# Performance work log

Measured on AMD Instinct MI355X. Metric: run time of the kernel, lower is better.

Reference implementation:

```python
import jax, jax.numpy as jnp
import numpy as np

NPAD = 50      # npadding from init
N_ITER = 5     # fixed Newton iteration count (torch uses tol-based early stop)
LR = 0.5


def conv_subspace(raw, kernel, npadding):
    # raw: (ntrial, nneuron, nt_full); kernel: (ntau, nsubspace)
    ntrial, nneuron, nt = raw.shape
    # enforce causality: prepend a zero tap
    k = jnp.concatenate([jnp.zeros((1, kernel.shape[1]), kernel.dtype), kernel], axis=0)
    ntau = k.shape[0]
    nfft = nt + ntau - 1
    Rf = jnp.fft.rfft(raw, n=nfft, axis=2)[..., None]          # (m, n, F, 1)
    Kf = jnp.fft.rfft(k, n=nfft, axis=0)[None, None, :, :]     # (1, 1, F, s)
    G = jnp.fft.irfft(Rf * Kf, n=nfft, axis=2)                 # (m, n, nfft, s)
    G = jnp.where(jnp.abs(G) < 1e-5, 0.0, G)                   # thresholding as in torch
    G = G[:, :, npadding:nt, :]                                # keep causal part, drop padding
    return jnp.swapaxes(G, -1, -2)                             # (m, n, s, T)


def setup_inputs() -> dict:
    key = jax.random.key(0)
    k1, k2, k3 = jax.random.split(key, 3)
    ntrial, nneuron, nt_full = 16, 96, 350
    T, nsub, ntau, nlat = 300, 8, 20, 8
    # spike counts
    Y_raw = jax.random.randint(k1, (ntrial, nneuron, nt_full), 0, 4).astype(jnp.float32)
    kernel = 0.02 * jax.random.normal(k2, (ntau, nsub), jnp.float32)
    w_proj = 0.05 * jax.random.normal(k3, (nsub, nlat), jnp.float32)
    # smooth RBF latent prior covariance (PSD, as a GP kernel K must be)
    t = jnp.arange(T, dtype=jnp.float32)
    K = jnp.exp(-(t[:, None] - t[None, :]) ** 2 / (2.0 * 20.0 ** 2))
    bias = jnp.float32(0.5)
    return {"Y_raw": Y_raw, "kernel": kernel, "w_proj": w_proj, "K": K, "bias": bias}


def reference(Y_raw, kernel, w_proj, K, bias):
    # FFT causal conv -> subspace signals -> per-neuron latent loading weights
    G = conv_subspace(Y_raw, kernel, NPAD)                     # (m, n, s, T)
    weights = jnp.einsum('mnst,sl->mnlt', G, w_proj)           # (m, n, L, T)
    Y = Y_raw[:, :, NPAD:]                                     # (m, n, T)
    m, n, L, T = weights.shape
    I = jnp.eye(T, dtype=K.dtype)
    inv_K = jnp.linalg.inv(K + 1e-3 * I)                       # (T, T)
    mu = jnp.zeros((m, L, T), Y.dtype)
    hessian = jnp.broadcast_to(inv_K, (m, L, T, T))            # torch init: +inv_K repeated
    w2 = weights ** 2
    for _ in range(N_ITER):
        log_lambd = jnp.einsum('mnlt,mlt->mnt', weights, mu) + bias
        h_inv = jnp.linalg.inv(hessian)                        # batched (m*L) TxT inverse
        dh = jnp.diagonal(h_inv, axis1=-2, axis2=-1)           # (m, L, T)
        lambd = jnp.exp(log_lambd + 0.5 * jnp.einsum('mlt,mnlt->mnt', dh, w2))
        grad = jnp.einsum('mnlt,mnt->mlt', weights, Y - lambd) - jnp.einsum('mlt,ts->mls', mu, inv_K)
        d = jnp.einsum('mnlt,mnt->mlt', w2, lambd)             # (m, L, T)
        hessian = -inv_K - d[..., :, None] * I                 # -inv_K - diag(d)
        mu = mu - LR * jnp.linalg.solve(hessian, grad[..., None])[..., 0]
    return mu
```

## Files before the change

kernel.cpp:

```cpp
#include <hip/hip_runtime.h>
#include <math.h>

namespace {
constexpr int Mb   = 16;
constexpr int Nn   = 96;
constexpr int NTF  = 350;
constexpr int Tt   = 300;
constexpr int NSUB = 8;
constexpr int NTAU = 20;
constexpr int NL   = 8;
constexpr int ML   = Mb * NL;
constexpr int R_   = 32;
constexpr int CS   = 33;
constexpr int CL   = 34;
constexpr int LDW  = 33;
constexpr int TP   = 320;
constexpr int CROWS= 384;
constexpr int NSIT = 12;
constexpr float EPS = 0.001f;
}

__device__ __forceinline__ int PIV(int k) { return (600 * k + 300) >> 6; }

__device__ __forceinline__ float  sqrt_(float x)  { return sqrtf(x); }
__device__ __forceinline__ double sqrt_(double x) { return sqrt(x); }

__device__ __forceinline__ void lfence() {
  asm volatile("s_waitcnt lgkmcnt(0)" ::: "memory");
}

template <typename T>
__device__ void chol32_trtri32(T* A, T* W, T* rd, T* V, int tid) {
  if (tid < 32) {
    const int r = tid;
    for (int c = 0; c < 32; ++c) {
      T dotp = (T)0, dotv = (T)0;
      for (int k = 0; k < c; ++k) {
        const T bc = A[c * LDW + k];
        dotp += bc * bc;
        dotv += A[r * LDW + k] * bc;
      }
      const T pivot = A[c * LDW + c] - dotp;
      T s, is;
      if (pivot > (T)1e-12) { s = sqrt_(pivot); is = (T)1 / s; }
      else                  { s = (T)0;         is = (T)0; }
      if (r == c)      { A[c * LDW + c] = s; rd[c] = is; }
      else if (r > c)  A[r * LDW + c] = (A[r * LDW + c] - dotv) * is;
      lfence();
    }
  }
  __syncthreads();
  if (tid < 32) {
    const int c = tid;
    V[c * LDW + c] = rd[c];
    for (int r = c + 1; r < 32; ++r) {
      T acc = (T)0;
      for (int k = c; k < r; ++k) acc += A[r * LDW + k] * V[k * LDW + c];
      V[r * LDW + c] = -acc * rd[r];
    }
    for (int r = 0; r < 32; ++r)
      W[r * LDW + c] = (r < c) ? (T)0 : V[r * LDW + c];
  }
  __syncthreads();
}

__global__ __launch_bounds__(256) void k_weights(
    const float* __restrict__ Yraw, const float* __restrict__ kern,
    const float* __restrict__ wproj, float* __restrict__ WA,
    float* __restrict__ Yt) {
  __shared__ float sk[NTAU * NSUB];
  __shared__ float sp[NSUB * NL];
  const int tid = threadIdx.x;
  if (tid < NTAU * NSUB) sk[tid] = kern[tid];
  if (tid < NSUB * NL)   sp[tid] = wproj[tid];
  __syncthreads();
  const int g = blockIdx.x * 256 + tid;
  if (g >= Mb * Tt * Nn) return;
  const int n  = g % Nn;
  const int mt = g / Nn;
  const int t  = mt % Tt;
  const int m  = mt / Tt;
  const float* yr = Yraw + ((size_t)m * Nn + n) * NTF + 30 + t;
  float ya[NTAU + 1];
#pragma unroll
  for (int j = 0; j <= NTAU; ++j) ya[j] = yr[j];
  float gs[NSUB];
#pragma unroll
  for (int s = 0; s < NSUB; ++s) {
    float acc = 0.f;
#pragma unroll
    for (int j = 0; j < NTAU; ++j) acc += ya[j] * sk[(NTAU - 1 - j) * NSUB + s];
    gs[s] = (fabsf(acc) < 1e-5f) ? 0.f : acc;
  }
  float w[NL];
#pragma unroll
  for (int l = 0; l < NL; ++l) {
    float acc = 0.f;
#pragma unroll
    for (int s = 0; s < NSUB; ++s) acc += gs[s] * sp[s * NL + l];
    w[l] = acc;
  }
  float4* wa4 = reinterpret_cast<float4*>(WA + (size_t)g * NL);
  wa4[0] = make_float4(w[0], w[1], w[2], w[3]);
  wa4[1] = make_float4(w[4], w[5], w[6], w[7]);
  Yt[g] = ya[NTAU];
}

__global__ __launch_bounds__(256) void k_scholM(
    const float* __restrict__ K, double* __restrict__ WS64) {
  __shared__ double A[R_ * LDW];
  __shared__ double V[R_ * LDW];
  __shared__ double rd[R_];
  const int tid = threadIdx.x;
  for (int e = tid; e < R_ * R_; e += 256) {
    const int a = e >> 5, b = e & 31;
    A[a * LDW + b] = (double)K[(size_t)PIV(a) * Tt + PIV(b)];
  }
  __syncthreads();
  chol32_trtri32<double>(A, WS64, rd, V, tid);
}

__global__ __launch_bounds__(320) void k_cmake(
    const float* __restrict__ K, const double* __restrict__ WS64,
    float* __restrict__ Cg) {
  const int k = blockIdx.x;
  const int t = threadIdx.x;
  if (k == R_) {
    for (int r = t; r < CROWS; r += 320) Cg[(size_t)r * CS + R_] = 0.f;
    return;
  }
  __shared__ double wrow[R_];
  if (t < R_) wrow[t] = WS64[(size_t)k * LDW + t];
  __syncthreads();
  if (t < Tt) {
    double acc = 0.0;
    for (int j = 0; j <= k; ++j)
      acc += wrow[j] * (double)K[(size_t)PIV(j) * Tt + t];
    Cg[(size_t)t * CS + k] = (float)acc;
  }
  for (int r = Tt + t; r < CROWS; r += 320) Cg[(size_t)r * CS + k] = 0.f;
}

__global__ __launch_bounds__(256) void k_rmul(
    const float* __restrict__ Cg, double* __restrict__ R64) {
  const int e = blockIdx.x * 256 + threadIdx.x;
  if (e >= R_ * R_) return;
  const int i = e >> 5, j = e & 31;
  double acc = (i == j) ? 0.001 : 0.0;
  for (int r = 0; r < Tt; ++r)
    acc += (double)Cg[(size_t)r * CS + i] * (double)Cg[(size_t)r * CS + j];
  R64[e] = acc;
}

__global__ __launch_bounds__(256) void k_qchol(
    const double* __restrict__ R64, double* __restrict__ W64) {
  __shared__ double A[R_ * LDW];
  __shared__ double V[R_ * LDW];
  __shared__ double rd[R_];
  const int tid = threadIdx.x;
  for (int e = tid; e < R_ * R_; e += 256) {
    const int i = e >> 5, j = e & 31;
    A[i * LDW + j] = R64[e];
  }
  __syncthreads();
  chol32_trtri32<double>(A, W64, rd, V, tid);
}

__global__ __launch_bounds__(256) void k_qmul(
    const double* __restrict__ W64, double* __restrict__ Qg) {
  const int e = blockIdx.x * 256 + threadIdx.x;
  if (e >= R_ * R_) return;
  const int i = e >> 5, j = e & 31;
  const int k0 = (i > j) ? i : j;
  double acc = 0.0;
  for (int k = k0; k < R_; ++k) acc += W64[k * LDW + i] * W64[k * LDW + j];
  Qg[e] = acc;
}

__global__ __launch_bounds__(256) void k_init(
    float* __restrict__ mu, float* __restrict__ dh) {
  const int g = blockIdx.x * 256 + threadIdx.x;
  if (g >= Mb * Tt * NL) return;
  mu[g] = 0.f;
  dh[g] = 1.0f + EPS;
}

__global__ __launch_bounds__(256) void k_gd2(
    const float* __restrict__ WA, const float* __restrict__ Yt,
    const float* __restrict__ mug, const float* __restrict__ dhg,
    const float* __restrict__ biasp, float* __restrict__ g1,
    float* __restrict__ dvec) {
  const int wg = blockIdx.x;
  const int m = wg / 10, ch = wg - m * 10;
  const int t0 = ch * 30;
  const int tid = threadIdx.x;
  __shared__ float pg[30 * 8 * 8];
  __shared__ float pd[30 * 8 * 8];
  if (tid < 240) {
    const int tl = tid >> 3, nq = tid & 7;
    const int t = t0 + tl;
    const float b = biasp[0];
    const float4* mp = reinterpret_cast<const float4*>(mug + ((size_t)m * Tt + t) * NL);
    const float4* dp = reinterpret_cast<const float4*>(dhg + ((size_t)m * Tt + t) * NL);
    const float4 m0 = mp[0], m1 = mp[1], h0 = dp[0], h1 = dp[1];
    const float mv[8] = {m0.x, m0.y, m0.z, m0.w, m1.x, m1.y, m1.z, m1.w};
    const float hv[8] = {0.5f * h0.x, 0.5f * h0.y, 0.5f * h0.z, 0.5f * h0.w,
                         0.5f * h1.x, 0.5f * h1.y, 0.5f * h1.z, 0.5f * h1.w};
    float ga[8], dd[8];
#pragma unroll
    for (int l = 0; l < 8; ++l) { ga[l] = 0.f; dd[l] = 0.f; }
    const float* war = WA + ((size_t)m * Tt + t) * Nn * NL;
    const float* ytr = Yt + ((size_t)m * Tt + t) * Nn;
    for (int i = 0; i < 12; ++i) {
      const int n = nq + 8 * i;
      const float4* w4 = reinterpret_cast<const float4*>(war + n * NL);
      const float4 w0 = w4[0], w1 = w4[1];
      const float wv[8] = {w0.x, w0.y, w0.z, w0.w, w1.x, w1.y, w1.z, w1.w};
      float e = b;
#pragma unroll
      for (int l = 0; l < 8; ++l) e += wv[l] * (mv[l] + wv[l] * hv[l]);
      const float lamn = expf(e);
      const float dy = ytr[n] - lamn;
#pragma unroll
      for (int l = 0; l < 8; ++l) {
        ga[l] += wv[l] * dy;
        dd[l] += wv[l] * wv[l] * lamn;
      }
    }
#pragma unroll
    for (int l = 0; l < 8; ++l) {
      pg[(tl * 8 + l) * 8 + nq] = ga[l];
      pd[(tl * 8 + l) * 8 + nq] = dd[l];
    }
  }
  __syncthreads();
  if (tid < 240) {
    const int tl = tid >> 3, l = tid & 7;
    float sg_ = 0.f, sd_ = 0.f;
#pragma unroll
    for (int nq = 0; nq < 8; ++nq) {
      sg_ += pg[(tl * 8 + l) * 8 + nq];
      sd_ += pd[(tl * 8 + l) * 8 + nq];
    }
    const size_t idx = (size_t)(m * NL + l) * TP + (t0 + tl);
    g1[idx]   = sg_;
    dvec[idx] = sd_;
  }
}

__global__ __launch_bounds__(320) void k_sys2(
    const float* __restrict__ Cg, const double* __restrict__ Qg,
    const float* __restrict__ g1, const float* __restrict__ dvec,
    float* __restrict__ mug, float* __restrict__ dhg) {
  const int ml = blockIdx.x;
  const int mt = ml / NL, lat = ml % NL;
  const int tid = threadIdx.x;
  __shared__ float  Cf[Tt * CL];
  __shared__ float  M[R_ * LDW];
  __shared__ float  Xa[R_ * LDW];
  __shared__ float  Xb[R_ * LDW];
  __shared__ float  T[R_ * LDW];
  __shared__ float  muv[Tt], gv[Tt], sv[Tt], dl[Tt], sg[Tt];
  __shared__ double pv[R_], qv[R_];
  __shared__ double pB[R_ * 10];
  __shared__ float  pU[R_ * 10];
  __shared__ float  uv[R_], yv[R_];
  __shared__ float  red[R_ + 2];
  for (int e = tid; e < Tt * CS; e += 320) {
    const int r = e / CS, c = e - r * CS;
    Cf[r * CL + c] = Cg[e];
  }
  if (tid < Tt) {
    const float m_ = mug[((size_t)mt * Tt + tid) * NL + lat];
    const float g_ = g1[(size_t)ml * TP + tid];
    const float d_ = dvec[(size_t)ml * TP + tid];
    muv[tid] = m_; gv[tid] = g_;
    const float s = 1.f / (1.f + EPS * d_);
    sv[tid] = s;
    dl[tid] = d_ * s;
  }
  __syncthreads();
  {
    const int k = tid & 31, ch = tid >> 5;
    double acc = 0.0;
    const int ta = ch * 30;
    for (int t = ta; t < ta + 30; ++t)
      acc += (double)Cf[t * CL + k] * (double)muv[t];
    pB[k * 10 + ch] = acc;
  }
  __syncthreads();
  if (tid < R_) {
    double a = 0.0;
    for (int ch = 0; ch < 10; ++ch) a += pB[tid * 10 + ch];
    pv[tid] = a;
  }
  __syncthreads();
  if (tid < R_) {
    double acc = 0.0;
    for (int j = 0; j < R_; ++j) acc += Qg[(size_t)j * R_ + tid] * pv[j];
    qv[tid] = acc;
  }
  __syncthreads();
  if (tid < Tt) {
    double cq = 0.0;
    for (int k = 0; k < R_; ++k) cq += (double)Cf[tid * CL + k] * qv[k];
    const double gnew = (double)gv[tid] - 1000.0 * ((double)muv[tid] - cq);
    gv[tid] = (float)gnew;
    sg[tid] = sv[tid] * (float)gnew;
  }
  __syncthreads();
  {
    const int k = tid & 31, ch = tid >> 5;
    float acc = 0.f;
    const int ta = ch * 30;
    for (int t = ta; t < ta + 30; ++t) acc += Cf[t * CL + k] * sg[t];
    pU[k * 10 + ch] = acc;
  }
  __syncthreads();
  if (tid < R_) {
    float a = 0.f;
    for (int ch = 0; ch < 10; ++ch) a += pU[tid * 10 + ch];
    uv[tid] = a;
  }
  if (tid < 256) {
    const int i0 = (tid >> 4) * 2, j0 = (tid & 15) * 2;
    float a00 = 0.f, a01 = 0.f, a10 = 0.f, a11 = 0.f;
    for (int t = 0; t < Tt; ++t) {
      const float w = dl[t];
      const float2 u = *reinterpret_cast<const float2*>(&Cf[t * CL + i0]);
      const float2 v = *reinterpret_cast<const float2*>(&Cf[t * CL + j0]);
      const float u0 = u.x * w, u1 = u.y * w;
      a00 += u0 * v.x; a01 += u0 * v.y;
      a10 += u1 * v.x; a11 += u1 * v.y;
    }
    M[(i0    ) * LDW + j0    ] = a00 + ((i0     == j0    ) ? 1.f : 0.f);
    M[(i0    ) * LDW + j0 + 1] = a01 + ((i0     == j0 + 1) ? 1.f : 0.f);
    M[(i0 + 1) * LDW + j0    ] = a10 + ((i0 + 1 == j0    ) ? 1.f : 0.f);
    M[(i0 + 1) * LDW + j0 + 1] = a11 + ((i0 + 1 == j0 + 1) ? 1.f : 0.f);
  }
  __syncthreads();
  if (tid < R_) {
    float rs = 0.f;
    for (int j = 0; j < R_; ++j) rs += fabsf(M[tid * LDW + j]);
    red[tid] = rs;
  }
  __syncthreads();
  if (tid == 0) {
    float g = 0.f;
    for (int i = 0; i < R_; ++i) g = fmaxf(g, red[i]);
    red[R_] = 1.f / g;
  }
  __syncthreads();
  {
    const float c0 = red[R_];
    for (int e = tid; e < R_ * R_; e += 320) {
      const int i = e >> 5, j = e & 31;
      Xa[i * LDW + j] = (i == j) ? c0 : 0.f;
    }
  }
  __syncthreads();
  float* Xc = Xa;
  float* Xn = Xb;
  {
    const int i = tid >> 3, j0 = (tid & 7) * 4;
    for (int it = 0; it < NSIT; ++it) {
      if (tid < 256) {
        float a0 = 0.f, a1 = 0.f, a2 = 0.f, a3 = 0.f;
        for (int k = 0; k < R_; ++k) {
          const float mv = M[i * LDW + k];
          const float* xr = &Xc[k * LDW + j0];
          a0 += mv * xr[0]; a1 += mv * xr[1]; a2 += mv * xr[2]; a3 += mv * xr[3];
        }
        float* tr = &T[i * LDW + j0];
        tr[0] = a0; tr[1] = a1; tr[2] = a2; tr[3] = a3;
      }
      __syncthreads();
      if (tid < 256) {
        float a0 = 0.f, a1 = 0.f, a2 = 0.f, a3 = 0.f;
        for (int k = 0; k < R_; ++k) {
          const float xv = Xc[i * LDW + k];
          const float* tr = &T[k * LDW + j0];
          a0 += xv * tr[0]; a1 += xv * tr[1]; a2 += xv * tr[2]; a3 += xv * tr[3];
        }
        const float* xc = &Xc[i * LDW + j0];
        float* xn = &Xn[i * LDW + j0];
        xn[0] = 2.f * xc[0] - a0; xn[1] = 2.f * xc[1] - a1;
        xn[2] = 2.f * xc[2] - a2; xn[3] = 2.f * xc[3] - a3;
      }
      __syncthreads();
      float* tmp = Xc; Xc = Xn; Xn = tmp;
    }
  }
  if (tid < R_) {
    float acc = 0.f;
    for (int j = 0; j < R_; ++j) acc += Xc[tid * LDW + j] * uv[j];
    yv[tid] = acc;
  }
  __syncthreads();
  if (tid < Tt) {
    const int t = tid;
    float cr[R_];
#pragma unroll
    for (int k = 0; k < R_; ++k) cr[k] = Cf[t * CL + k];
    float q = 0.f, cy = 0.f;
    for (int j = 0; j < R_; ++j) {
      float x = 0.f;
#pragma unroll
      for (int k = 0; k < R_; ++k) x += cr[k] * Xc[k * LDW + j];
      q += x * cr[j];
    }
#pragma unroll
    for (int k = 0; k < R_; ++k) cy += cr[k] * yv[k];
    const float s = sv[t];
    const size_t idx = ((size_t)mt * Tt + t) * NL + lat;
    const float x2 = EPS * s * gv[t] + s * cy;
    mug[idx] = muv[t] + 0.5f * x2;
    dhg[idx] = -(EPS * s + s * s * q);
  }
}

__global__ __launch_bounds__(256) void k_out(
    const float* __restrict__ mu, float* __restrict__ out) {
  const int g = blockIdx.x * 256 + threadIdx.x;
  if (g >= Mb * NL * Tt) return;
  const int t = g % Tt;
  const int ml = g / Tt;
  const int m = ml / NL, l = ml % NL;
  out[g] = mu[((size_t)m * Tt + t) * NL + l];
}

extern "C" void kernel_launch(void* const* d_in, const int* in_sizes, int n_in,
                              void* d_out, int out_size, void* d_ws, size_t ws_size,
                              hipStream_t stream) {
  (void)in_sizes; (void)n_in; (void)out_size;
  const float* Yraw  = (const float*)d_in[0];
  const float* kern  = (const float*)d_in[1];
  const float* wproj = (const float*)d_in[2];
  const float* K     = (const float*)d_in[3];
  const float* biasp = (const float*)d_in[4];
  float* out = (float*)d_out;

  char* base = (char*)d_ws;
  size_t off = 0;
  auto alloc = [&](size_t bytes) -> void* {
    void* p = base + off;
    off += (bytes + 511) & ~(size_t)511;
    return p;
  };
  float*  WA   = (float*) alloc((size_t)Mb * Tt * Nn * NL * 4);
  float*  Yt   = (float*) alloc((size_t)Mb * Tt * Nn * 4);
  float*  mu   = (float*) alloc((size_t)Mb * Tt * NL * 4);
  float*  dh   = (float*) alloc((size_t)Mb * Tt * NL * 4);
  float*  g1   = (float*) alloc((size_t)ML * TP * 4);
  float*  dvec = (float*) alloc((size_t)ML * TP * 4);
  float*  Cg   = (float*) alloc((size_t)CROWS * CS * 4);
  double* WS64 = (double*)alloc((size_t)R_ * LDW * 8);
  double* W64  = (double*)alloc((size_t)R_ * LDW * 8);
  double* R64  = (double*)alloc((size_t)R_ * R_ * 8);
  double* Q64  = (double*)alloc((size_t)R_ * R_ * 8);
  if (off > ws_size) return;

  const int gMTN = (Mb * Tt * Nn) / 256;
  const int gMTL = (Mb * Tt * NL + 255) / 256;
  const int gRR  = (R_ * R_ + 255) / 256;

  k_weights<<<gMTN, 256, 0, stream>>>(Yraw, kern, wproj, WA, Yt);
  k_scholM<<<1, 256, 0, stream>>>(K, WS64);
  k_cmake<<<R_ + 1, 320, 0, stream>>>(K, WS64, Cg);
  k_rmul<<<gRR, 256, 0, stream>>>(Cg, R64);
  k_qchol<<<1, 256, 0, stream>>>(R64, W64);
  k_qmul<<<gRR, 256, 0, stream>>>(W64, Q64);
  k_init<<<gMTL, 256, 0, stream>>>(mu, dh);

  for (int it = 0; it < 5; ++it) {
    k_gd2<<<Mb * 10, 256, 0, stream>>>(WA, Yt, mu, dh, biasp, g1, dvec);
    k_sys2<<<ML, 320, 0, stream>>>(Cg, Q64, g1, dvec, mu, dh);
  }
  k_out<<<gMTL, 256, 0, stream>>>(mu, out);
}
```

Baseline: 339.0 us.

## Retile k_sys2 matmuls into 4x4 register blocks with single-wave Newton-Schulz

Pads shared-memory row strides to 36 so float4 loads are aligned, and retiles the Gram-matrix build into 4x4 register tiles split over four time chunks, reduced through a scratch buffer. The Newton-Schulz inverse iterations now run on one 64-thread wavefront using 4x4 tiles, with LDS waitcnt fences in place of block barriers. The quadratic-form diagonal is computed with 4x4 tiles spread across all threads, and Q is staged into shared memory. This cuts LDS traffic and barrier count, but leaves most of the block idle during the iterative inverse and uses more shared memory, which may lower occupancy. The iteration relies on M being symmetric, since it reads M column-wise.

```diff
diff --git a/kernel.cpp b/kernel.cpp
--- a/kernel.cpp
+++ b/kernel.cpp
@@ -12,8 +12,8 @@
 constexpr int ML   = Mb * NL;
 constexpr int R_   = 32;
 constexpr int CS   = 33;
-constexpr int CL   = 34;
-constexpr int LDW  = 33;
+constexpr int CL   = 36;
+constexpr int LDW  = 36;
 constexpr int TP   = 320;
 constexpr int CROWS= 384;
 constexpr int NSIT = 12;
@@ -260,16 +260,19 @@
   __shared__ float  Xa[R_ * LDW];
   __shared__ float  Xb[R_ * LDW];
   __shared__ float  T[R_ * LDW];
+  __shared__ float  scratch[4096];
   __shared__ float  muv[Tt], gv[Tt], sv[Tt], dl[Tt], sg[Tt];
+  __shared__ double Qs[R_ * R_];
   __shared__ double pv[R_], qv[R_];
   __shared__ double pB[R_ * 10];
   __shared__ float  pU[R_ * 10];
   __shared__ float  uv[R_], yv[R_];
-  __shared__ float  red[R_ + 2];
+  __shared__ float  redg[R_ + 2];
   for (int e = tid; e < Tt * CS; e += 320) {
     const int r = e / CS, c = e - r * CS;
     Cf[r * CL + c] = Cg[e];
   }
+  for (int e = tid; e < R_ * R_; e += 320) Qs[e] = Qg[e];
   if (tid < Tt) {
     const float m_ = mug[((size_t)mt * Tt + tid) * NL + lat];
     const float g_ = g1[(size_t)ml * TP + tid];
@@ -297,7 +300,7 @@
   __syncthreads();
   if (tid < R_) {
     double acc = 0.0;
-    for (int j = 0; j < R_; ++j) acc += Qg[(size_t)j * R_ + tid] * pv[j];
+    for (int j = 0; j < R_; ++j) acc += Qs[j * R_ + tid] * pv[j];
     qv[tid] = acc;
   }
   __syncthreads();
@@ -323,98 +326,166 @@
     uv[tid] = a;
   }
   if (tid < 256) {
-    const int i0 = (tid >> 4) * 2, j0 = (tid & 15) * 2;
-    float a00 = 0.f, a01 = 0.f, a10 = 0.f, a11 = 0.f;
-    for (int t = 0; t < Tt; ++t) {
+    const int ch = tid >> 6, til = tid & 63;
+    const int i0 = (til >> 3) * 4, j0 = (til & 7) * 4;
+    float acc[4][4];
+#pragma unroll
+    for (int r = 0; r < 4; ++r)
+#pragma unroll
+      for (int c = 0; c < 4; ++c) acc[r][c] = 0.f;
+    const int ta = ch * 75, tb = ta + 75;
+    for (int t = ta; t < tb; ++t) {
       const float w = dl[t];
-      const float2 u = *reinterpret_cast<const float2*>(&Cf[t * CL + i0]);
-      const float2 v = *reinterpret_cast<const float2*>(&Cf[t * CL + j0]);
-      const float u0 = u.x * w, u1 = u.y * w;
-      a00 += u0 * v.x; a01 += u0 * v.y;
-      a10 += u1 * v.x; a11 += u1 * v.y;
-    }
-    M[(i0    ) * LDW + j0    ] = a00 + ((i0     == j0    ) ? 1.f : 0.f);
-    M[(i0    ) * LDW + j0 + 1] = a01 + ((i0     == j0 + 1) ? 1.f : 0.f);
-    M[(i0 + 1) * LDW + j0    ] = a10 + ((i0 + 1 == j0    ) ? 1.f : 0.f);
-    M[(i0 + 1) * LDW + j0 + 1] = a11 + ((i0 + 1 == j0 + 1) ? 1.f : 0.f);
+      const float4 u = *reinterpret_cast<const float4*>(&Cf[t * CL + i0]);
+      const float4 v = *reinterpret_cast<const float4*>(&Cf[t * CL + j0]);
+      const float ua[4] = {u.x * w, u.y * w, u.z * w, u.w * w};
+      const float vb[4] = {v.x, v.y, v.z, v.w};
+#pragma unroll
+      for (int r = 0; r < 4; ++r)
+#pragma unroll
+        for (int c = 0; c < 4; ++c) acc[r][c] += ua[r] * vb[c];
+    }
+    float* p = &scratch[(ch * 64 + til) * 16];
+#pragma unroll
+    for (int r = 0; r < 4; ++r)
+#pragma unroll
+      for (int c = 0; c < 4; ++c) p[r * 4 + c] = acc[r][c];
+  }
+  __syncthreads();
+  for (int e = tid; e < R_ * R_; e += 320) {
+    const int i = e >> 5, j = e & 31;
+    const int til = (i >> 2) * 8 + (j >> 2);
+    const int el = (i & 3) * 4 + (j & 3);
+    const float val = scratch[(0 * 64 + til) * 16 + el] + scratch[(1 * 64 + til) * 16 + el]
+                    + scratch[(2 * 64 + til) * 16 + el] + scratch[(3 * 64 + til) * 16 + el];
+    M[i * LDW + j] = val + ((i == j) ? 1.f : 0.f);
   }
   __syncthreads();
   if (tid < R_) {
     float rs = 0.f;
     for (int j = 0; j < R_; ++j) rs += fabsf(M[tid * LDW + j]);
-    red[tid] = rs;
+    redg[tid] = rs;
   }
   __syncthreads();
   if (tid == 0) {
     float g = 0.f;
-    for (int i = 0; i < R_; ++i) g = fmaxf(g, red[i]);
-    red[R_] = 1.f / g;
+    for (int i = 0; i < R_; ++i) g = fmaxf(g, redg[i]);
+    redg[R_] = 1.f / g;
   }
   __syncthreads();
   {
-    const float c0 = red[R_];
+    const float c0 = redg[R_];
     for (int e = tid; e < R_ * R_; e += 320) {
       const int i = e >> 5, j = e & 31;
       Xa[i * LDW + j] = (i == j) ? c0 : 0.f;
     }
   }
   __syncthreads();
-  float* Xc = Xa;
-  float* Xn = Xb;
-  {
-    const int i = tid >> 3, j0 = (tid & 7) * 4;
+  if (tid < 64) {
+    const int i0 = (tid >> 3) * 4, j0 = (tid & 7) * 4;
+    float* Xc = Xa;
+    float* Xn = Xb;
     for (int it = 0; it < NSIT; ++it) {
-      if (tid < 256) {
-        float a0 = 0.f, a1 = 0.f, a2 = 0.f, a3 = 0.f;
+      {
+        float acc[4][4];
+#pragma unroll
+        for (int r = 0; r < 4; ++r)
+#pragma unroll
+          for (int c = 0; c < 4; ++c) acc[r][c] = 0.f;
         for (int k = 0; k < R_; ++k) {
-          const float mv = M[i * LDW + k];
-          const float* xr = &Xc[k * LDW + j0];
-          a0 += mv * xr[0]; a1 += mv * xr[1]; a2 += mv * xr[2]; a3 += mv * xr[3];
+          const float4 m4 = *reinterpret_cast<const float4*>(&M[k * LDW + i0]);
+          const float4 x4 = *reinterpret_cast<const float4*>(&Xc[k * LDW + j0]);
+          const float ma[4] = {m4.x, m4.y, m4.z, m4.w};
+          const float xb4[4] = {x4.x, x4.y, x4.z, x4.w};
+#pragma unroll
+          for (int r = 0; r < 4; ++r)
+#pragma unroll
+            for (int c = 0; c < 4; ++c) acc[r][c] += ma[r] * xb4[c];
         }
-        float* tr = &T[i * LDW + j0];
-        tr[0] = a0; tr[1] = a1; tr[2] = a2; tr[3] = a3;
+#pragma unroll
+        for (int r = 0; r < 4; ++r)
+          *reinterpret_cast<float4*>(&T[(i0 + r) * LDW + j0]) =
+              make_float4(acc[r][0], acc[r][1], acc[r][2], acc[r][3]);
       }
-      __syncthreads();
-      if (tid < 256) {
-        float a0 = 0.f, a1 = 0.f, a2 = 0.f, a3 = 0.f;
+      lfence();
+      {
+        float acc[4][4];
+#pragma unroll
+        for (int r = 0; r < 4; ++r)
+#pragma unroll
+          for (int c = 0; c < 4; ++c) acc[r][c] = 0.f;
         for (int k = 0; k < R_; ++k) {
-          const float xv = Xc[i * LDW + k];
-          const float* tr = &T[k * LDW + j0];
-          a0 += xv * tr[0]; a1 += xv * tr[1]; a2 += xv * tr[2]; a3 += xv * tr[3];
+          const float4 x4 = *reinterpret_cast<const float4*>(&Xc[k * LDW + i0]);
+          const float4 t4 = *reinterpret_cast<const float4*>(&T[k * LDW + j0]);
+          const float xa4[4] = {x4.x, x4.y, x4.z, x4.w};
+          const float tb4[4] = {t4.x, t4.y, t4.z, t4.w};
+#pragma unroll
+          for (int r = 0; r < 4; ++r)
+#pragma unroll
+            for (int c = 0; c < 4; ++c) acc[r][c] += xa4[r] * tb4[c];
         }
-        const float* xc = &Xc[i * LDW + j0];
-        float* xn = &Xn[i * LDW + j0];
-        xn[0] = 2.f * xc[0] - a0; xn[1] = 2.f * xc[1] - a1;
-        xn[2] = 2.f * xc[2] - a2; xn[3] = 2.f * xc[3] - a3;
+#pragma unroll
+        for (int r = 0; r < 4; ++r) {
+          const float4 xc4 = *reinterpret_cast<const float4*>(&Xc[(i0 + r) * LDW + j0]);
+          *reinterpret_cast<float4*>(&Xn[(i0 + r) * LDW + j0]) =
+              make_float4(2.f * xc4.x - acc[r][0], 2.f * xc4.y - acc[r][1],
+                          2.f * xc4.z - acc[r][2], 2.f * xc4.w - acc[r][3]);
+        }
       }
-      __syncthreads();
+      lfence();
       float* tmp = Xc; Xc = Xn; Xn = tmp;
     }
   }
+  __syncthreads();
   if (tid < R_) {
     float acc = 0.f;
-    for (int j = 0; j < R_; ++j) acc += Xc[tid * LDW + j] * uv[j];
+    for (int j = 0; j < R_; ++j) acc += Xa[tid * LDW + j] * uv[j];
     yv[tid] = acc;
   }
   __syncthreads();
+  float* redq = scratch;
+  for (int tix = tid; tix < 600; tix += 320) {
+    const int ig = tix & 7, tg = tix >> 3;
+    const int t0 = tg * 4, i0 = ig * 4;
+    float acc[4][4];
+#pragma unroll
+    for (int r = 0; r < 4; ++r)
+#pragma unroll
+      for (int c = 0; c < 4; ++c) acc[r][c] = 0.f;
+    for (int k = 0; k < R_; ++k) {
+      const float4 p4 = *reinterpret_cast<const float4*>(&Xa[k * LDW + i0]);
+      const float pa[4] = {p4.x, p4.y, p4.z, p4.w};
+      const float cr0 = Cf[(t0 + 0) * CL + k];
+      const float cr1 = Cf[(t0 + 1) * CL + k];
+      const float cr2 = Cf[(t0 + 2) * CL + k];
+      const float cr3 = Cf[(t0 + 3) * CL + k];
+#pragma unroll
+      for (int c = 0; c < 4; ++c) {
+        acc[0][c] += cr0 * pa[c];
+        acc[1][c] += cr1 * pa[c];
+        acc[2][c] += cr2 * pa[c];
+        acc[3][c] += cr3 * pa[c];
+      }
+    }
+#pragma unroll
+    for (int r = 0; r < 4; ++r) {
+      const float4 c4 = *reinterpret_cast<const float4*>(&Cf[(t0 + r) * CL + i0]);
+      const float qp = acc[r][0] * c4.x + acc[r][1] * c4.y
+                     + acc[r][2] * c4.z + acc[r][3] * c4.w;
+      redq[(t0 + r) * 8 + ig] = qp;
+    }
+  }
+  __syncthreads();
   if (tid < Tt) {
-    const int t = tid;
-    float cr[R_];
-#pragma unroll
-    for (int k = 0; k < R_; ++k) cr[k] = Cf[t * CL + k];
-    float q = 0.f, cy = 0.f;
-    for (int j = 0; j < R_; ++j) {
-      float x = 0.f;
-#pragma unroll
-      for (int k = 0; k < R_; ++k) x += cr[k] * Xc[k * LDW + j];
-      q += x * cr[j];
-    }
-#pragma unroll
-    for (int k = 0; k < R_; ++k) cy += cr[k] * yv[k];
-    const float s = sv[t];
-    const size_t idx = ((size_t)mt * Tt + t) * NL + lat;
-    const float x2 = EPS * s * gv[t] + s * cy;
-    mug[idx] = muv[t] + 0.5f * x2;
+    float q = 0.f;
+#pragma unroll
+    for (int g = 0; g < 8; ++g) q += redq[tid * 8 + g];
+    float cy = 0.f;
+    for (int k = 0; k < R_; ++k) cy += Cf[tid * CL + k] * yv[k];
+    const float s = sv[tid];
+    const size_t idx = ((size_t)mt * Tt + tid) * NL + lat;
+    const float x2 = EPS * s * gv[tid] + s * cy;
+    mug[idx] = muv[tid] + 0.5f * x2;
     dhg[idx] = -(EPS * s + s * s * q);
   }
 }
```

Measured after the change: 347.3 us. 1.02x slower.
